# Kernel tuning notes

Measured on AMD Instinct MI355X. Metric: run time of the kernel, lower is better.

Reference implementation:

```python
import jax, jax.numpy as jnp
import numpy as np

B, S, H, D, AD = 64, 200, 4, 256, 256  # batch, max_len, heads, hidden, attribute hidden
HD = D // H  # head dim 64
LN_EPS = 1e-12

PARAM_SHAPES = [
    ('Wq', (D, D)), ('bq', (D,)), ('Wk', (D, D)), ('bk', (D,)), ('Wv', (D, D)), ('bv', (D,)),
    ('Wqp', (D, D)), ('bqp', (D,)), ('Wkp', (D, D)), ('bkp', (D,)),
    ('Waq', (AD, AD)), ('baq', (AD,)), ('Wak', (AD, AD)), ('bak', (AD,)), ('Wav', (AD, AD)), ('bav', (AD,)),
    ('Wqic', (D, AD)), ('bqic', (AD,)), ('Wqci', (AD, D)), ('bqci', (D,)),
    ('Wqpc', (D, AD)), ('bqpc', (AD,)), ('Wqcp', (AD, D)), ('bqcp', (D,)),
    ('Wf1', (S, S)), ('bf1', (S,)), ('Wf2', (S, 1)), ('bf2', (1,)),
    ('Wd', (D, D)), ('bd', (D,)), ('ln_g', (D,)), ('ln_b', (D,)),
    ('Wda', (AD, AD)), ('bda', (AD,)), ('lna_g', (AD,)), ('lna_b', (AD,)),
]


def setup_inputs() -> dict:
    key = jax.random.key(0)
    ks = jax.random.split(key, 8 + len(PARAM_SHAPES))
    inp = {
        'input_tensor': jax.random.normal(ks[0], (B, S, D), jnp.float32),
        'attribute_table': jax.random.normal(ks[1], (1, B, S, 1, AD), jnp.float32),
        'position_embedding': jax.random.normal(ks[2], (B, S, D), jnp.float32),
        'hidden_state_attr': jax.random.normal(ks[3], (1, B, S, 1, AD), jnp.float32),
        'attention_mask': jnp.zeros((B, 1, S, S), jnp.float32),
        'fusion_w': jax.random.uniform(ks[4], (9,), jnp.float32),
        'fusion_wc': jax.random.uniform(ks[5], (4,), jnp.float32),
    }
    for j, (name, shp) in enumerate(PARAM_SHAPES):
        if name.startswith('ln') or name == 'lna_g':
            inp[name] = jnp.ones(shp, jnp.float32) if name.endswith('_g') else jnp.zeros(shp, jnp.float32)
        else:
            inp[name] = jax.random.normal(ks[8 + j], shp, jnp.float32) * 0.02
    return inp


def _forward(input_tensor, attribute_table, position_embedding, hidden_state_attr,
             attention_mask, fusion_w, fusion_wc,
             Wq, bq, Wk, bk, Wv, bv, Wqp, bqp, Wkp, bkp,
             Waq, baq, Wak, bak, Wav, bav, Wqic, bqic, Wqci, bqci,
             Wqpc, bqpc, Wqcp, bqcp, Wf1, bf1, Wf2, bf2,
             Wd, bd, ln_g, ln_b, Wda, bda, lna_g, lna_b):
    lin = lambda x, W, b: x @ W + b

    def heads(x):  # [B,S,D] -> [B,H,S,hd]
        b_, s_, _ = x.shape
        return x.reshape(b_, s_, H, -1).transpose(0, 2, 1, 3)

    def ln(x, g, b):
        m = x.mean(-1, keepdims=True)
        v = ((x - m) ** 2).mean(-1, keepdims=True)
        return (x - m) / jnp.sqrt(v + LN_EPS) * g + b

    attr = attribute_table[0, :, :, 0, :]      # [B,S,AD] (squeeze(-2), feat 0)
    hattr = hidden_state_attr[0, :, :, 0, :]   # [B,S,AD]

    iq, ik, iv = heads(lin(input_tensor, Wq, bq)), heads(lin(input_tensor, Wk, bk)), heads(lin(input_tensor, Wv, bv))
    pq, pk = heads(lin(position_embedding, Wqp, bqp)), heads(lin(position_embedding, Wkp, bkp))
    aq, ak = heads(lin(attr, Waq, baq)), heads(lin(attr, Wak, bak))
    haq, hak, hav = heads(lin(hattr, Waq, baq)), heads(lin(hattr, Wak, bak)), heads(lin(hattr, Wav, bav))
    iqc = heads(lin(input_tensor, Wqic, bqic))
    ciq = heads(lin(attr, Wqci, bqci))
    cqp = heads(lin(attr, Wqcp, bqcp))
    cqp_a = heads(lin(hattr, Wqcp, bqcp))
    pqc = heads(lin(position_embedding, Wqpc, bqpc))

    sc = lambda q, k: jnp.einsum('bhid,bhjd->bhij', q, k)
    pp = sc(pq, pk)
    # 9 item-side streams: ii, ic, ip, ci, cc, cp, pi, pc, pp (matches torch append order)
    raw = jnp.stack([sc(iq, ik), sc(iqc, ak), sc(iq, pk), sc(ciq, ik), sc(aq, ak),
                     sc(cqp, pk), sc(pq, ik), sc(pqc, ak), pp], axis=1)   # [B,9,H,S,S]
    raw_c = jnp.stack([sc(haq, hak), sc(cqp_a, pk), sc(pqc, hak), pp], axis=1)  # [B,4,H,S,S]

    def gate(x, fw):  # VanillaAttention(max_len, max_len) over stream axis
        x = jnp.transpose(x, (0, 2, 3, 1, 4)) * fw[:, None]  # [B,H,S,C,S]
        e = (jax.nn.relu(x @ Wf1 + bf1) @ Wf2 + bf2)[..., 0]  # [B,H,S,C]
        w = jax.nn.softmax(e, axis=-1)
        return jnp.einsum('bhscj,bhsc->bhsj', x, w)  # [B,H,S,S]

    scale = 1.0 / np.sqrt(HD)

    def attend(a, v):
        p = jax.nn.softmax(a * scale + attention_mask, axis=-1)
        ctx = jnp.einsum('bhij,bhjd->bhid', p, v)
        b_ = ctx.shape[0]
        return ctx.transpose(0, 2, 1, 3).reshape(b_, S, -1)

    ctx = attend(gate(raw, fusion_w), iv)
    ctx_c = attend(gate(raw_c, fusion_wc), hav)
    hidden_states = ln(ctx @ Wd + bd + input_tensor, ln_g, ln_b)
    hidden_states_attr = ln(ctx_c @ Wda + bda + hattr, lna_g, lna_b)
    return hidden_states, hidden_states_attr


def reference(input_tensor, attribute_table, position_embedding, hidden_state_attr,
              attention_mask, fusion_w, fusion_wc,
              Wq, bq, Wk, bk, Wv, bv, Wqp, bqp, Wkp, bkp,
              Waq, baq, Wak, bak, Wav, bav, Wqic, bqic, Wqci, bqci,
              Wqpc, bqpc, Wqcp, bqcp, Wf1, bf1, Wf2, bf2,
              Wd, bd, ln_g, ln_b, Wda, bda, lna_g, lna_b):
    return _forward(input_tensor, attribute_table, position_embedding, hidden_state_attr,
                    attention_mask, fusion_w, fusion_wc,
                    Wq, bq, Wk, bk, Wv, bv, Wqp, bqp, Wkp, bkp,
                    Waq, baq, Wak, bak, Wav, bav, Wqic, bqic, Wqci, bqci,
                    Wqpc, bqpc, Wqcp, bqcp, Wf1, bf1, Wf2, bf2,
                    Wd, bd, ln_g, ln_b, Wda, bda, lna_g, lna_b)
```

## Files before the change

kernel.cpp:

```cpp
#include <hip/hip_runtime.h>
#include <cstddef>

typedef __attribute__((ext_vector_type(8))) short bf16x8;
typedef __attribute__((ext_vector_type(4))) short bf16x4;
typedef __attribute__((ext_vector_type(4))) float f32x4;

constexpr int Bc = 64;
constexpr int Sc = 200;
constexpr int Hc = 4;
constexpr int Dc = 256;
constexpr int HDc = 64;
constexpr int NPc = Bc * Sc;
constexpr int NPROJ = 15;
constexpr int NWT   = 17;
constexpr float SCALE = 0.125f;


__constant__ int c_KP9[3]  = {1,6,4};
__constant__ int c_QP9[9]  = {0,11,3, 10,5,14, 0,12,3};
__constant__ int c_CG9[9]  = {0,3,6, 1,4,7, 2,5,8};
__constant__ int c_M2S9[9] = {0,24,48,8,32,56,16,40,64};
__constant__ int c_KP4[2]  = {8,4};
__constant__ int c_QP4[4]  = {7,14, 13,3};
__constant__ int c_CG4[4]  = {0,2, 1,3};
__constant__ int c_M2S4[4] = {0,16,8,24};

__device__ __forceinline__ short f2bf(float x) {
    union { float f; unsigned u; } v; v.f = x;
    unsigned r = v.u + 0x7FFFu + ((v.u >> 16) & 1u);
    return (short)(r >> 16);
}
__device__ __forceinline__ float bf2f(short x) {
    union { unsigned u; float f; } v; v.u = ((unsigned)(unsigned short)x) << 16;
    return v.f;
}
__device__ __forceinline__ f32x4 mfma16(bf16x8 a, bf16x8 b, f32x4 c) {
    return __builtin_amdgcn_mfma_f32_16x16x32_bf16(a, b, c, 0, 0, 0);
}

struct ProjArgsM {
    const short* A[NPROJ];
    const float* bias[NPROJ];
};
struct WList { const float* w[NWT]; };

__global__ void cast_in(const float* __restrict__ s0, const float* __restrict__ s1,
                        const float* __restrict__ s2, const float* __restrict__ s3,
                        short* __restrict__ dst) {
    const float* srcs[4] = {s0, s1, s2, s3};
    const float* src = srcs[blockIdx.y];
    short* d = dst + (size_t)blockIdx.y * NPc * Dc;
    int t = blockIdx.x * 256 + threadIdx.x;
    float4 v = ((const float4*)src)[t];
    bf16x4 o;
    o[0] = f2bf(v.x); o[1] = f2bf(v.y); o[2] = f2bf(v.z); o[3] = f2bf(v.w);
    *(bf16x4*)(d + (size_t)t * 4) = o;
}

__global__ void cast_wt(WList wl, short* __restrict__ dst) {
    __shared__ float tbuf[64][65];
    const int p = blockIdx.y;
    const int k0 = (blockIdx.x >> 2) * 64, n0 = (blockIdx.x & 3) * 64;
    const float* W = wl.w[p];
    short* d = dst + (size_t)p * Dc * Dc;
    const int tid = threadIdx.x;
    for (int i = tid; i < 64 * 64; i += 256) {
        int k = i >> 6, n = i & 63;
        tbuf[k][n] = W[(size_t)(k0 + k) * Dc + n0 + n];
    }
    __syncthreads();
    for (int i = tid; i < 64 * 64; i += 256) {
        int n = i >> 6, k = i & 63;
        d[(size_t)(n0 + n) * Dc + k0 + k] = f2bf(tbuf[k][n]);
    }
}

__global__ void wf1t_kernel(const float* __restrict__ Wf1, short* __restrict__ WT) {
    int t = blockIdx.x * 256 + threadIdx.x;
    if (t < 224 * 224) {
        int j = t / 224, i = t % 224;
        WT[t] = (i < Sc && j < Sc) ? f2bf(Wf1[(size_t)i * Sc + j]) : (short)0;
    }
}

__global__ __launch_bounds__(256) void vt_kernel(const short* __restrict__ proj_bf,
                                                 short* __restrict__ vt) {
    const int bid = blockIdx.x;
    const int t  = bid >> 8;
    const int bh = bid & 255;
    const int b = bh >> 2, h = bh & 3;
    const int p = t ? 9 : 2;
    const short* src = proj_bf + ((size_t)p * NPc + (size_t)b * Sc) * Dc + h * HDc;
    short* dst = vt + ((size_t)t * 256 + bh) * 64 * 224;
    __shared__ short tile[200][72];
    const int tid = threadIdx.x;
    for (int idx = tid; idx < 200 * 8; idx += 256) {
        int j = idx >> 3, c8 = idx & 7;
        *(bf16x8*)(&tile[j][c8 * 8]) = *(const bf16x8*)(src + (size_t)j * Dc + c8 * 8);
    }
    __syncthreads();
    for (int idx = tid; idx < 64 * 28; idx += 256) {
        int d = idx / 28, c8 = idx % 28;
        bf16x8 o;
        #pragma unroll
        for (int i = 0; i < 8; ++i) {
            int j = c8 * 8 + i;
            o[i] = (j < 200) ? tile[j][d] : (short)0;
        }
        *(bf16x8*)(dst + (size_t)d * 224 + c8 * 8) = o;
    }
}

__global__ __launch_bounds__(256, 4) void proj_mfma(
    ProjArgsM args, const short* __restrict__ WTall, short* __restrict__ proj_bf)
{
    const int p  = blockIdx.y;
    const int m0 = blockIdx.x * 64;
    const short* __restrict__ A   = args.A[p];
    const short* __restrict__ WTp = WTall + (size_t)p * Dc * Dc;
    const float* __restrict__ bias = args.bias[p];
    short* __restrict__ ob = proj_bf + (size_t)p * NPc * Dc;

    __shared__ __align__(16) short As[64 * 264];
    const int tid = threadIdx.x;
    const int lane = tid & 63, w = tid >> 6;
    const int l15 = lane & 15, l4 = lane >> 4;

    for (int t = tid; t < 64 * 32; t += 256) {
        int r = t >> 5, c8 = t & 31;
        *(bf16x8*)(As + r * 264 + c8 * 8) = *(const bf16x8*)(A + (size_t)(m0 + r) * Dc + c8 * 8);
    }
    __syncthreads();

    f32x4 acc[4][4];
    #pragma unroll
    for (int mi = 0; mi < 4; ++mi)
        #pragma unroll
        for (int ni = 0; ni < 4; ++ni) acc[mi][ni] = (f32x4){};

    const int nb = w * 64;
    #pragma unroll
    for (int ks = 0; ks < 8; ++ks) {
        bf16x8 bfr[4];
        #pragma unroll
        for (int ni = 0; ni < 4; ++ni)
            bfr[ni] = *(const bf16x8*)(WTp + (size_t)(nb + ni * 16 + l15) * Dc + ks * 32 + l4 * 8);
        #pragma unroll
        for (int mi = 0; mi < 4; ++mi) {
            bf16x8 a = *(const bf16x8*)(As + (mi * 16 + l15) * 264 + ks * 32 + l4 * 8);
            #pragma unroll
            for (int ni = 0; ni < 4; ++ni)
                acc[mi][ni] = mfma16(a, bfr[ni], acc[mi][ni]);
        }
    }

    float bv[4];
    #pragma unroll
    for (int ni = 0; ni < 4; ++ni) bv[ni] = bias[nb + ni * 16 + l15];
    #pragma unroll
    for (int mi = 0; mi < 4; ++mi) {
        #pragma unroll
        for (int ni = 0; ni < 4; ++ni) {
            int n = nb + ni * 16 + l15;
            #pragma unroll
            for (int i = 0; i < 4; ++i) {
                int m = m0 + mi * 16 + l4 * 4 + i;
                ob[(size_t)m * Dc + n] = f2bf(acc[mi][ni][i] + bv[ni]);
            }
        }
    }
}

template <int CH, int NG, int CPG, int QT, int MT2>
__device__ void fused_body(
    int bid,
    const short* __restrict__ proj_bf,
    const short* __restrict__ vtb,
    const float* __restrict__ fw,
    const float* __restrict__ mask,
    const short* __restrict__ WT,
    const float* __restrict__ bf1,
    const float* __restrict__ Wf2,
    short* __restrict__ ctx_out,
    const int* KP, const int* QP, const int* CG, const int* M2S,
    short* Sl, float* gbuf, float* evw, float* fwl,
    float* bf1l, float* wf2l)
{
    constexpr int GR    = CPG * 8;
    constexpr int VROWS = NG * GR;
    constexpr int SROWS = MT2 * 16;
    constexpr int SLD   = 232;
    constexpr int NW    = 4;

    const int tid = threadIdx.x;
    const int rt  = bid % 25;
    const int h   = (bid / 25) & 3;
    const int b   = bid / 100;
    const int r0  = rt * 8;
    const int lane = tid & 63, wv = tid >> 6;
    const int l15 = lane & 15, l4 = lane >> 4;
    const int brow0 = b * Sc + r0;

    {
        bf16x8 z = {};
        if constexpr (SROWS > VROWS) {
            for (int t = tid; t < (SROWS - VROWS) * 28; t += 256) {
                int r = VROWS + t / 28, c8 = t % 28;
                *(bf16x8*)(Sl + r * SLD + c8 * 8) = z;
            }
        }
        for (int t = tid; t < VROWS * 3; t += 256) {
            int r = t / 3, c8 = t % 3;
            *(bf16x8*)(Sl + r * SLD + 200 + c8 * 8) = z;
        }
    }
    if (tid < 224) {
        bf1l[tid] = (tid < Sc) ? bf1[tid] : 0.f;
        wf2l[tid] = (tid < Sc) ? Wf2[tid] : 0.f;
    }
    if (tid < CH) fwl[tid] = fw[tid];

    bf16x8 af[NG][QT][2];
    #pragma unroll
    for (int g = 0; g < NG; ++g) {
        #pragma unroll
        for (int t = 0; t < QT; ++t) {
            int sr = t * 16 + l15;
            int kk = (sr < GR) ? (sr >> 3) : 0;
            int rr = (sr < GR) ? (sr & 7) : 0;
            const short* qp = proj_bf + ((size_t)QP[g * CPG + kk] * NPc + brow0 + rr) * Dc + h * HDc;
            #pragma unroll
            for (int ks = 0; ks < 2; ++ks)
                af[g][t][ks] = *(const bf16x8*)(qp + ks * 32 + l4 * 8);
        }
    }
    __syncthreads();

    {
        const short* Kb[NG];
        #pragma unroll
        for (int g = 0; g < NG; ++g)
            Kb[g] = proj_bf + ((size_t)KP[g] * NPc + (size_t)b * Sc) * Dc + h * HDc;

        float fwv[NG][QT];
        #pragma unroll
        for (int g = 0; g < NG; ++g)
            #pragma unroll
            for (int t = 0; t < QT; ++t) {
                int k = t * 2 + (l4 >> 1);
                fwv[g][t] = (k < CPG) ? fwl[CG[g * CPG + k]] : 0.f;
            }

        bf16x8 cur[NG][2];
        int nt = wv;
        {
            int j = nt * 16 + l15;
            #pragma unroll
            for (int g = 0; g < NG; ++g) {
                cur[g][0] = *(const bf16x8*)(Kb[g] + (size_t)j * Dc + l4 * 8);
                cur[g][1] = *(const bf16x8*)(Kb[g] + (size_t)j * Dc + 32 + l4 * 8);
            }
        }
        while (nt < 13) {
            const int ntn = nt + NW;
            bf16x8 nxt[NG][2];
            if (ntn < 13) {
                int j2 = ntn * 16 + l15;
                #pragma unroll
                for (int g = 0; g < NG; ++g) {
                    nxt[g][0] = *(const bf16x8*)(Kb[g] + (size_t)j2 * Dc + l4 * 8);
                    nxt[g][1] = *(const bf16x8*)(Kb[g] + (size_t)j2 * Dc + 32 + l4 * 8);
                }
            }
            const int j = nt * 16 + l15;
            const bool jv = (j < Sc);
            #pragma unroll
            for (int g = 0; g < NG; ++g) {
                #pragma unroll
                for (int t = 0; t < QT; ++t) {
                    f32x4 c = {};
                    c = mfma16(af[g][t][0], cur[g][0], c);
                    c = mfma16(af[g][t][1], cur[g][1], c);
                    int k = t * 2 + (l4 >> 1);
                    if (jv && k < CPG) {
                        int srb = g * GR + t * 16 + l4 * 4;
                        float f = fwv[g][t];
                        #pragma unroll
                        for (int i = 0; i < 4; ++i)
                            Sl[(srb + i) * SLD + j] = f2bf(c[i] * f);
                    }
                }
            }
            #pragma unroll
            for (int g = 0; g < NG; ++g) { cur[g][0] = nxt[g][0]; cur[g][1] = nxt[g][1]; }
            nt = ntn;
        }
    }
    __syncthreads();

    {
        float epart[MT2];
        #pragma unroll
        for (int mt = 0; mt < MT2; ++mt) epart[mt] = 0.f;

        for (int nt = wv; nt < 13; nt += NW) {
            const int jr = nt * 16 + l15;
            bf16x8 wfrag[7];
            #pragma unroll
            for (int ks = 0; ks < 7; ++ks)
                wfrag[ks] = *(const bf16x8*)(WT + (size_t)jr * 224 + ks * 32 + l4 * 8);
            f32x4 cg[MT2];
            #pragma unroll
            for (int mt = 0; mt < MT2; ++mt) cg[mt] = (f32x4){};
            #pragma unroll
            for (int ks = 0; ks < 7; ++ks) {
                #pragma unroll
                for (int mt = 0; mt < MT2; ++mt) {
                    bf16x8 bb = *(const bf16x8*)(Sl + (mt * 16 + l15) * SLD + ks * 32 + l4 * 8);
                    cg[mt] = mfma16(wfrag[ks], bb, cg[mt]);
                }
            }
            float4 b1 = *(const float4*)(bf1l + nt * 16 + l4 * 4);
            float4 w2 = *(const float4*)(wf2l + nt * 16 + l4 * 4);
            #pragma unroll
            for (int mt = 0; mt < MT2; ++mt) {
                float s = fmaxf(cg[mt][0] + b1.x, 0.f) * w2.x
                        + fmaxf(cg[mt][1] + b1.y, 0.f) * w2.y
                        + fmaxf(cg[mt][2] + b1.z, 0.f) * w2.z
                        + fmaxf(cg[mt][3] + b1.w, 0.f) * w2.w;
                s += __shfl_xor(s, 16, 64);
                s += __shfl_xor(s, 32, 64);
                epart[mt] += s;
            }
        }
        if (l4 == 0) {
            #pragma unroll
            for (int mt = 0; mt < MT2; ++mt)
                evw[wv * SROWS + mt * 16 + l15] = epart[mt];
        }
    }
    __syncthreads();

    const int ra = wv, rb = wv + 4;

    float wchA[CH], wchB[CH];
    {
        float eA[CH], eB[CH];
        float mxA = -1e30f, mxB = -1e30f;
        #pragma unroll
        for (int c = 0; c < CH; ++c) {
            int m = M2S[c];
            float sA = 0.f, sB = 0.f;
            #pragma unroll
            for (int w = 0; w < NW; ++w) {
                sA += evw[w * SROWS + m + ra];
                sB += evw[w * SROWS + m + rb];
            }
            eA[c] = sA; eB[c] = sB;
            mxA = fmaxf(mxA, sA); mxB = fmaxf(mxB, sB);
        }
        float suA = 0.f, suB = 0.f;
        #pragma unroll
        for (int c = 0; c < CH; ++c) {
            eA[c] = __expf(eA[c] - mxA); suA += eA[c];
            eB[c] = __expf(eB[c] - mxB); suB += eB[c];
        }
        float ivA = 1.f / suA, ivB = 1.f / suB;
        #pragma unroll
        for (int c = 0; c < CH; ++c) { wchA[c] = eA[c] * ivA; wchB[c] = eB[c] * ivB; }
    }

    if (lane < 50) {
        const int j4 = lane * 4;
        const float* mbase = mask + ((size_t)b * Sc + r0) * Sc;
        float aA[4] = {0.f, 0.f, 0.f, 0.f};
        float aB[4] = {0.f, 0.f, 0.f, 0.f};
        #pragma unroll
        for (int c = 0; c < CH; ++c) {
            bf16x4 sA = *(const bf16x4*)(Sl + (M2S[c] + ra) * SLD + j4);
            bf16x4 sB = *(const bf16x4*)(Sl + (M2S[c] + rb) * SLD + j4);
            float wA = wchA[c], wB = wchB[c];
            #pragma unroll
            for (int i = 0; i < 4; ++i) {
                aA[i] += wA * bf2f(sA[i]);
                aB[i] += wB * bf2f(sB[i]);
            }
        }
        float4 mA = *(const float4*)(mbase + (size_t)ra * Sc + j4);
        float4 mB = *(const float4*)(mbase + (size_t)rb * Sc + j4);
        float4 oA = make_float4(aA[0] * SCALE + mA.x, aA[1] * SCALE + mA.y,
                                aA[2] * SCALE + mA.z, aA[3] * SCALE + mA.w);
        float4 oB = make_float4(aB[0] * SCALE + mB.x, aB[1] * SCALE + mB.y,
                                aB[2] * SCALE + mB.z, aB[3] * SCALE + mB.w);
        *(float4*)(gbuf + ra * 200 + j4) = oA;
        *(float4*)(gbuf + rb * 200 + j4) = oB;
    }

    #pragma unroll
    for (int rr = 0; rr < 2; ++rr) {
        const int r = wv + rr * 4;
        float vals[4]; float mpart = -1e30f;
        #pragma unroll
        for (int t4 = 0; t4 < 4; ++t4) {
            int j = t4 * 64 + lane;
            vals[t4] = (j < Sc) ? gbuf[r * 200 + j] : -1e30f;
            mpart = fmaxf(mpart, vals[t4]);
        }
        #pragma unroll
        for (int off = 32; off >= 1; off >>= 1) mpart = fmaxf(mpart, __shfl_xor(mpart, off, 64));
        float pv[4]; float spart = 0.f;
        #pragma unroll
        for (int t4 = 0; t4 < 4; ++t4) {
            int j = t4 * 64 + lane;
            pv[t4] = (j < Sc) ? __expf(vals[t4] - mpart) : 0.f;
            spart += pv[t4];
        }
        #pragma unroll
        for (int off = 32; off >= 1; off >>= 1) spart += __shfl_xor(spart, off, 64);
        float inv = 1.f / spart;
        #pragma unroll
        for (int t4 = 0; t4 < 4; ++t4) {
            int j = t4 * 64 + lane;
            if (j < Sc) Sl[r * SLD + j] = f2bf(pv[t4] * inv);
        }
    }
    __syncthreads();

    {
        const short* vb = vtb + ((size_t)(b * Hc + h) * 64) * 224;
        const int nb = wv * 16;
        f32x4 c0 = {}, c1 = {};
        #pragma unroll
        for (int ks = 0; ks < 7; ks += 2) {
            bf16x8 aa = *(const bf16x8*)(Sl + l15 * SLD + ks * 32 + l4 * 8);
            bf16x8 bb = *(const bf16x8*)(vb + (size_t)(nb + l15) * 224 + ks * 32 + l4 * 8);
            c0 = mfma16(aa, bb, c0);
            if (ks + 1 < 7) {
                bf16x8 aa1 = *(const bf16x8*)(Sl + l15 * SLD + (ks + 1) * 32 + l4 * 8);
                bf16x8 bb1 = *(const bf16x8*)(vb + (size_t)(nb + l15) * 224 + (ks + 1) * 32 + l4 * 8);
                c1 = mfma16(aa1, bb1, c1);
            }
        }
        if (l4 < 2) {
            #pragma unroll
            for (int i = 0; i < 4; ++i) {
                int row = l4 * 4 + i;
                ctx_out[((size_t)(brow0 + row)) * Dc + h * HDc + nb + l15] =
                    f2bf(c0[i] + c1[i]);
            }
        }
    }
}

__global__ __launch_bounds__(256, 3) void fused7(
    const short* __restrict__ proj_bf,
    const short* __restrict__ vt,
    const float* __restrict__ fw9,
    const float* __restrict__ fw4,
    const float* __restrict__ mask,
    const short* __restrict__ WT,
    const float* __restrict__ bf1,
    const float* __restrict__ Wf2,
    short* __restrict__ ctxb,
    short* __restrict__ ctxcb)
{
    __shared__ __align__(16) short Sl[80 * 232];
    __shared__ float gbuf[8 * 200];
    __shared__ float evw[4 * 80];
    __shared__ float fwl[9];
    __shared__ float bf1l[224];
    __shared__ float wf2l[224];

    const int d    = blockIdx.x;
    const int xcd  = d & 7;
    const int slot = d >> 3;
    const int chunk = (slot / 25) * 8 + xcd;
    const int pos   = slot % 25;
    const int bid   = chunk * 25 + pos;

    if (bid < 6400) {
        fused_body<9, 3, 3, 2, 5>(bid, proj_bf, vt, fw9, mask, WT, bf1, Wf2, ctxb,
                                  c_KP9, c_QP9, c_CG9, c_M2S9,
                                  Sl, gbuf, evw, fwl, bf1l, wf2l);
    } else {
        fused_body<4, 2, 2, 1, 2>(bid - 6400, proj_bf, vt + (size_t)256 * 64 * 224,
                                  fw4, mask, WT, bf1, Wf2, ctxcb,
                                  c_KP4, c_QP4, c_CG4, c_M2S4,
                                  Sl, gbuf, evw, fwl, bf1l, wf2l);
    }
}

__global__ __launch_bounds__(256, 3) void out_ln_mfma(
    const short* __restrict__ Ab,
    const short* __restrict__ WTp,
    const float* __restrict__ bias,
    const float* __restrict__ resid,
    const float* __restrict__ gamma,
    const float* __restrict__ beta,
    float* __restrict__ out)
{
    const int m0 = blockIdx.x * 32;
    __shared__ __align__(16) short As[32 * 264];
    __shared__ float ylds[32][257];
    const int tid = threadIdx.x;
    const int lane = tid & 63, wv = tid >> 6;
    const int l15 = lane & 15, l4 = lane >> 4;

    for (int t = tid; t < 32 * 32; t += 256) {
        int r = t >> 5, c8 = t & 31;
        *(bf16x8*)(As + r * 264 + c8 * 8) = *(const bf16x8*)(Ab + (size_t)(m0 + r) * Dc + c8 * 8);
    }
    __syncthreads();

    const int nb = wv * 64;
    f32x4 acc[2][4];
    #pragma unroll
    for (int mi = 0; mi < 2; ++mi)
        #pragma unroll
        for (int ni = 0; ni < 4; ++ni) acc[mi][ni] = (f32x4){};

    #pragma unroll
    for (int ks = 0; ks < 8; ++ks) {
        bf16x8 bfr[4];
        #pragma unroll
        for (int ni = 0; ni < 4; ++ni)
            bfr[ni] = *(const bf16x8*)(WTp + (size_t)(nb + ni * 16 + l15) * Dc + ks * 32 + l4 * 8);
        #pragma unroll
        for (int mi = 0; mi < 2; ++mi) {
            bf16x8 a = *(const bf16x8*)(As + (mi * 16 + l15) * 264 + ks * 32 + l4 * 8);
            #pragma unroll
            for (int ni = 0; ni < 4; ++ni)
                acc[mi][ni] = mfma16(a, bfr[ni], acc[mi][ni]);
        }
    }

    #pragma unroll
    for (int mi = 0; mi < 2; ++mi) {
        #pragma unroll
        for (int ni = 0; ni < 4; ++ni) {
            int n = nb + ni * 16 + l15;
            float bv = bias[n];
            #pragma unroll
            for (int i = 0; i < 4; ++i) {
                int row = mi * 16 + l4 * 4 + i;
                ylds[row][n] = acc[mi][ni][i] + bv + resid[(size_t)(m0 + row) * Dc + n];
            }
        }
    }
    __syncthreads();

    for (int r = wv * 8; r < wv * 8 + 8; ++r) {
        float v4[4];
        float s = 0.f, s2 = 0.f;
        #pragma unroll
        for (int t4 = 0; t4 < 4; ++t4) {
            float v = ylds[r][t4 * 64 + lane];
            v4[t4] = v;
            s += v; s2 += v * v;
        }
        #pragma unroll
        for (int off = 32; off >= 1; off >>= 1) {
            s  += __shfl_xor(s, off, 64);
            s2 += __shfl_xor(s2, off, 64);
        }
        float m   = s * (1.f / 256.f);
        float var = s2 * (1.f / 256.f) - m * m;
        float rstd = rsqrtf(var + 1e-12f);
        #pragma unroll
        for (int t4 = 0; t4 < 4; ++t4) {
            int ccol = t4 * 64 + lane;
            out[(size_t)(m0 + r) * Dc + ccol] = (v4[t4] - m) * rstd * gamma[ccol] + beta[ccol];
        }
    }
}

extern "C" void kernel_launch(void* const* d_in, const int* in_sizes, int n_in,
                              void* d_out, int out_size, void* d_ws, size_t ws_size,
                              hipStream_t stream) {
    const float* X    = (const float*)d_in[0];
    const float* AT   = (const float*)d_in[1];
    const float* P    = (const float*)d_in[2];
    const float* HA   = (const float*)d_in[3];
    const float* mask = (const float*)d_in[4];
    const float* fw   = (const float*)d_in[5];
    const float* fwc  = (const float*)d_in[6];

    const float* Wq   = (const float*)d_in[7];
    const float* bq   = (const float*)d_in[8];
    const float* Wk   = (const float*)d_in[9];
    const float* bk   = (const float*)d_in[10];
    const float* Wv   = (const float*)d_in[11];
    const float* bv   = (const float*)d_in[12];
    const float* Wqp  = (const float*)d_in[13];
    const float* bqp  = (const float*)d_in[14];
    const float* Wkp  = (const float*)d_in[15];
    const float* bkp  = (const float*)d_in[16];
    const float* Waq  = (const float*)d_in[17];
    const float* baq  = (const float*)d_in[18];
    const float* Wak  = (const float*)d_in[19];
    const float* bak  = (const float*)d_in[20];
    const float* Wav  = (const float*)d_in[21];
    const float* bav  = (const float*)d_in[22];
    const float* Wqic = (const float*)d_in[23];
    const float* bqic = (const float*)d_in[24];
    const float* Wqci = (const float*)d_in[25];
    const float* bqci = (const float*)d_in[26];
    const float* Wqpc = (const float*)d_in[27];
    const float* bqpc = (const float*)d_in[28];
    const float* Wqcp = (const float*)d_in[29];
    const float* bqcp = (const float*)d_in[30];
    const float* Wf1  = (const float*)d_in[31];
    const float* bf1  = (const float*)d_in[32];
    const float* Wf2  = (const float*)d_in[33];
    const float* bf2  = (const float*)d_in[34];
    const float* Wd   = (const float*)d_in[35];
    const float* bd   = (const float*)d_in[36];
    const float* ln_g = (const float*)d_in[37];
    const float* ln_b = (const float*)d_in[38];
    const float* Wda  = (const float*)d_in[39];
    const float* bda  = (const float*)d_in[40];
    const float* lna_g= (const float*)d_in[41];
    const float* lna_b= (const float*)d_in[42];

    char* w = (char*)d_ws;
    short* proj_bf = (short*)w;  w += (size_t)NPROJ * NPc * Dc * sizeof(short);
    short* WTall   = (short*)w;  w += (size_t)NWT * Dc * Dc * sizeof(short);
    short* WTf1    = (short*)w;  w += (size_t)224 * 224 * sizeof(short);
    short* inb     = (short*)w;  w += (size_t)4 * NPc * Dc * sizeof(short);
    short* vt      = (short*)w;  w += (size_t)2 * 256 * 64 * 224 * sizeof(short);
    short* ctxb    = (short*)w;  w += (size_t)NPc * Dc * sizeof(short);
    short* ctxcb   = (short*)w;  w += (size_t)NPc * Dc * sizeof(short);

    const int aid[NPROJ] = {0,0,0,2,2,1,1,3,3,3,0,1,1,3,2};
    const float* Wmat[NWT] = {Wq, Wk, Wv, Wqp, Wkp, Waq, Wak, Waq, Wak, Wav,
                              Wqic, Wqci, Wqcp, Wqcp, Wqpc, Wd, Wda};
    const float* bmat[NPROJ] = {bq, bk, bv, bqp, bkp, baq, bak, baq, bak, bav,
                                bqic, bqci, bqcp, bqcp, bqpc};

    ProjArgsM pm;
    WList wl;
    for (int i = 0; i < NPROJ; i++) {
        pm.A[i]    = inb + (size_t)aid[i] * NPc * Dc;
        pm.bias[i] = bmat[i];
    }
    for (int i = 0; i < NWT; i++) wl.w[i] = Wmat[i];

    cast_in<<<dim3(NPc * Dc / 4 / 256, 4), 256, 0, stream>>>(X, AT, P, HA, inb);
    cast_wt<<<dim3(16, NWT), 256, 0, stream>>>(wl, WTall);
    wf1t_kernel<<<(224 * 224 + 255) / 256, 256, 0, stream>>>(Wf1, WTf1);

    proj_mfma<<<dim3(NPc / 64, NPROJ), 256, 0, stream>>>(pm, WTall, proj_bf);

    vt_kernel<<<512, 256, 0, stream>>>(proj_bf, vt);

    fused7<<<12800, 256, 0, stream>>>(proj_bf, vt, fw, fwc, mask, WTf1, bf1, Wf2, ctxb, ctxcb);

    float* out0 = (float*)d_out;
    float* out1 = out0 + (size_t)NPc * Dc;
    out_ln_mfma<<<NPc / 32, 256, 0, stream>>>(ctxb,  WTall + (size_t)15 * Dc * Dc, bd,
                                              X,  ln_g,  ln_b,  out0);
    out_ln_mfma<<<NPc / 32, 256, 0, stream>>>(ctxcb, WTall + (size_t)16 * Dc * Dc, bda,
                                              HA, lna_g, lna_b, out1);
}
```

Before: 477.6 us.

## Cut fused attention LDS footprint and compute softmax in registers

Removes the gbuf and evw shared buffers from the fused attention kernel. The per-wave partial sums now go into the padding columns of the score tile, and the softmax runs directly on the register values each lane already holds instead of being staged through shared memory. The kernel's launch bounds are raised from 3 to 4 blocks per CU to use the smaller LDS footprint. It also replaces scalar bf16 rounding with the packed v_cvt_pk_bf16_f32 instruction in several kernels, which trades the hand-written rounding for the hardware conversion's rounding and risks register spills under the tighter bound.

New measurement: 594.1 us. 1.24x slower.

```diff
diff --git a/kernel.cpp b/kernel.cpp
--- a/kernel.cpp
+++ b/kernel.cpp
@@ -13,6 +13,7 @@
 constexpr int NPc = Bc * Sc;
 constexpr int NPROJ = 15;
 constexpr int NWT   = 17;
+constexpr int SLD   = 232;
 constexpr float SCALE = 0.125f;
 
 
@@ -34,6 +35,11 @@
     union { unsigned u; float f; } v; v.u = ((unsigned)(unsigned short)x) << 16;
     return v.f;
 }
+__device__ __forceinline__ unsigned cvtpk(float lo, float hi) {
+    unsigned r;
+    asm("v_cvt_pk_bf16_f32 %0, %1, %2" : "=v"(r) : "v"(lo), "v"(hi));
+    return r;
+}
 __device__ __forceinline__ f32x4 mfma16(bf16x8 a, bf16x8 b, f32x4 c) {
     return __builtin_amdgcn_mfma_f32_16x16x32_bf16(a, b, c, 0, 0, 0);
 }
@@ -52,9 +58,9 @@
     short* d = dst + (size_t)blockIdx.y * NPc * Dc;
     int t = blockIdx.x * 256 + threadIdx.x;
     float4 v = ((const float4*)src)[t];
-    bf16x4 o;
-    o[0] = f2bf(v.x); o[1] = f2bf(v.y); o[2] = f2bf(v.z); o[3] = f2bf(v.w);
-    *(bf16x4*)(d + (size_t)t * 4) = o;
+    unsigned p01 = cvtpk(v.x, v.y), p23 = cvtpk(v.z, v.w);
+    uint2 st; st.x = p01; st.y = p23;
+    *(uint2*)(d + (size_t)t * 4) = st;
 }
 
 __global__ void cast_wt(WList wl, short* __restrict__ dst) {
@@ -162,11 +168,13 @@
         #pragma unroll
         for (int ni = 0; ni < 4; ++ni) {
             int n = nb + ni * 16 + l15;
-            #pragma unroll
-            for (int i = 0; i < 4; ++i) {
-                int m = m0 + mi * 16 + l4 * 4 + i;
-                ob[(size_t)m * Dc + n] = f2bf(acc[mi][ni][i] + bv[ni]);
-            }
+            int m = m0 + mi * 16 + l4 * 4;
+            unsigned p01 = cvtpk(acc[mi][ni][0] + bv[ni], acc[mi][ni][1] + bv[ni]);
+            unsigned p23 = cvtpk(acc[mi][ni][2] + bv[ni], acc[mi][ni][3] + bv[ni]);
+            ob[(size_t)(m + 0) * Dc + n] = (short)p01;
+            ob[(size_t)(m + 1) * Dc + n] = (short)(p01 >> 16);
+            ob[(size_t)(m + 2) * Dc + n] = (short)p23;
+            ob[(size_t)(m + 3) * Dc + n] = (short)(p23 >> 16);
         }
     }
 }
@@ -183,13 +191,11 @@
     const float* __restrict__ Wf2,
     short* __restrict__ ctx_out,
     const int* KP, const int* QP, const int* CG, const int* M2S,
-    short* Sl, float* gbuf, float* evw, float* fwl,
-    float* bf1l, float* wf2l)
+    short* Sl, float* fwl, float* bf1l, float* wf2l)
 {
     constexpr int GR    = CPG * 8;
     constexpr int VROWS = NG * GR;
     constexpr int SROWS = MT2 * 16;
-    constexpr int SLD   = 232;
     constexpr int NW    = 4;
 
     const int tid = threadIdx.x;
@@ -285,9 +291,12 @@
                     if (jv && k < CPG) {
                         int srb = g * GR + t * 16 + l4 * 4;
                         float f = fwv[g][t];
-                        #pragma unroll
-                        for (int i = 0; i < 4; ++i)
-                            Sl[(srb + i) * SLD + j] = f2bf(c[i] * f);
+                        unsigned p01 = cvtpk(c[0] * f, c[1] * f);
+                        unsigned p23 = cvtpk(c[2] * f, c[3] * f);
+                        Sl[(srb + 0) * SLD + j] = (short)p01;
+                        Sl[(srb + 1) * SLD + j] = (short)(p01 >> 16);
+                        Sl[(srb + 2) * SLD + j] = (short)p23;
+                        Sl[(srb + 3) * SLD + j] = (short)(p23 >> 16);
                     }
                 }
             }
@@ -336,7 +345,7 @@
         if (l4 == 0) {
             #pragma unroll
             for (int mt = 0; mt < MT2; ++mt)
-                evw[wv * SROWS + mt * 16 + l15] = epart[mt];
+                *(float*)(Sl + (size_t)(mt * 16 + l15) * SLD + 224 + wv * 2) = epart[mt];
         }
     }
     __syncthreads();
@@ -353,8 +362,8 @@
             float sA = 0.f, sB = 0.f;
             #pragma unroll
             for (int w = 0; w < NW; ++w) {
-                sA += evw[w * SROWS + m + ra];
-                sB += evw[w * SROWS + m + rb];
+                sA += *(const float*)(Sl + (size_t)(m + ra) * SLD + 224 + w * 2);
+                sB += *(const float*)(Sl + (size_t)(m + rb) * SLD + 224 + w * 2);
             }
             eA[c] = sA; eB[c] = sB;
             mxA = fmaxf(mxA, sA); mxB = fmaxf(mxB, sB);
@@ -370,15 +379,17 @@
         for (int c = 0; c < CH; ++c) { wchA[c] = eA[c] * ivA; wchB[c] = eB[c] * ivB; }
     }
 
-    if (lane < 50) {
-        const int j4 = lane * 4;
+    const bool act = lane < 50;
+    const int j4 = lane * 4;
+    float vA[4], vB[4];
+    if (act) {
         const float* mbase = mask + ((size_t)b * Sc + r0) * Sc;
         float aA[4] = {0.f, 0.f, 0.f, 0.f};
         float aB[4] = {0.f, 0.f, 0.f, 0.f};
         #pragma unroll
         for (int c = 0; c < CH; ++c) {
-            bf16x4 sA = *(const bf16x4*)(Sl + (M2S[c] + ra) * SLD + j4);
-            bf16x4 sB = *(const bf16x4*)(Sl + (M2S[c] + rb) * SLD + j4);
+            bf16x4 sA = *(const bf16x4*)(Sl + (size_t)(M2S[c] + ra) * SLD + j4);
+            bf16x4 sB = *(const bf16x4*)(Sl + (size_t)(M2S[c] + rb) * SLD + j4);
             float wA = wchA[c], wB = wchB[c];
             #pragma unroll
             for (int i = 0; i < 4; ++i) {
@@ -388,40 +399,51 @@
         }
         float4 mA = *(const float4*)(mbase + (size_t)ra * Sc + j4);
         float4 mB = *(const float4*)(mbase + (size_t)rb * Sc + j4);
-        float4 oA = make_float4(aA[0] * SCALE + mA.x, aA[1] * SCALE + mA.y,
-                                aA[2] * SCALE + mA.z, aA[3] * SCALE + mA.w);
-        float4 oB = make_float4(aB[0] * SCALE + mB.x, aB[1] * SCALE + mB.y,
-                                aB[2] * SCALE + mB.z, aB[3] * SCALE + mB.w);
-        *(float4*)(gbuf + ra * 200 + j4) = oA;
-        *(float4*)(gbuf + rb * 200 + j4) = oB;
-    }
-
-    #pragma unroll
-    for (int rr = 0; rr < 2; ++rr) {
-        const int r = wv + rr * 4;
-        float vals[4]; float mpart = -1e30f;
-        #pragma unroll
-        for (int t4 = 0; t4 < 4; ++t4) {
-            int j = t4 * 64 + lane;
-            vals[t4] = (j < Sc) ? gbuf[r * 200 + j] : -1e30f;
-            mpart = fmaxf(mpart, vals[t4]);
-        }
-        #pragma unroll
-        for (int off = 32; off >= 1; off >>= 1) mpart = fmaxf(mpart, __shfl_xor(mpart, off, 64));
-        float pv[4]; float spart = 0.f;
-        #pragma unroll
-        for (int t4 = 0; t4 < 4; ++t4) {
-            int j = t4 * 64 + lane;
-            pv[t4] = (j < Sc) ? __expf(vals[t4] - mpart) : 0.f;
-            spart += pv[t4];
-        }
-        #pragma unroll
-        for (int off = 32; off >= 1; off >>= 1) spart += __shfl_xor(spart, off, 64);
-        float inv = 1.f / spart;
-        #pragma unroll
-        for (int t4 = 0; t4 < 4; ++t4) {
-            int j = t4 * 64 + lane;
-            if (j < Sc) Sl[r * SLD + j] = f2bf(pv[t4] * inv);
+        vA[0] = aA[0] * SCALE + mA.x; vA[1] = aA[1] * SCALE + mA.y;
+        vA[2] = aA[2] * SCALE + mA.z; vA[3] = aA[3] * SCALE + mA.w;
+        vB[0] = aB[0] * SCALE + mB.x; vB[1] = aB[1] * SCALE + mB.y;
+        vB[2] = aB[2] * SCALE + mB.z; vB[3] = aB[3] * SCALE + mB.w;
+    } else {
+        #pragma unroll
+        for (int i = 0; i < 4; ++i) { vA[i] = -1e30f; vB[i] = -1e30f; }
+    }
+
+    {
+        float mx = fmaxf(fmaxf(vA[0], vA[1]), fmaxf(vA[2], vA[3]));
+        #pragma unroll
+        for (int off = 32; off >= 1; off >>= 1) mx = fmaxf(mx, __shfl_xor(mx, off, 64));
+        float p0 = act ? __expf(vA[0] - mx) : 0.f;
+        float p1 = act ? __expf(vA[1] - mx) : 0.f;
+        float p2 = act ? __expf(vA[2] - mx) : 0.f;
+        float p3 = act ? __expf(vA[3] - mx) : 0.f;
+        float s = p0 + p1 + p2 + p3;
+        #pragma unroll
+        for (int off = 32; off >= 1; off >>= 1) s += __shfl_xor(s, off, 64);
+        float inv = 1.f / s;
+        if (act) {
+            uint2 st;
+            st.x = cvtpk(p0 * inv, p1 * inv);
+            st.y = cvtpk(p2 * inv, p3 * inv);
+            *(uint2*)(Sl + (size_t)ra * SLD + j4) = st;
+        }
+    }
+    {
+        float mx = fmaxf(fmaxf(vB[0], vB[1]), fmaxf(vB[2], vB[3]));
+        #pragma unroll
+        for (int off = 32; off >= 1; off >>= 1) mx = fmaxf(mx, __shfl_xor(mx, off, 64));
+        float p0 = act ? __expf(vB[0] - mx) : 0.f;
+        float p1 = act ? __expf(vB[1] - mx) : 0.f;
+        float p2 = act ? __expf(vB[2] - mx) : 0.f;
+        float p3 = act ? __expf(vB[3] - mx) : 0.f;
+        float s = p0 + p1 + p2 + p3;
+        #pragma unroll
+        for (int off = 32; off >= 1; off >>= 1) s += __shfl_xor(s, off, 64);
+        float inv = 1.f / s;
+        if (act) {
+            uint2 st;
+            st.x = cvtpk(p0 * inv, p1 * inv);
+            st.y = cvtpk(p2 * inv, p3 * inv);
+            *(uint2*)(Sl + (size_t)rb * SLD + j4) = st;
         }
     }
     __syncthreads();
@@ -452,7 +474,7 @@
     }
 }
 
-__global__ __launch_bounds__(256, 3) void fused7(
+__global__ __launch_bounds__(256, 4) void fused8(
     const short* __restrict__ proj_bf,
     const short* __restrict__ vt,
     const float* __restrict__ fw9,
@@ -464,9 +486,7 @@
     short* __restrict__ ctxb,
     short* __restrict__ ctxcb)
 {
-    __shared__ __align__(16) short Sl[80 * 232];
-    __shared__ float gbuf[8 * 200];
-    __shared__ float evw[4 * 80];
+    __shared__ __align__(16) short Sl[80 * SLD];
     __shared__ float fwl[9];
     __shared__ float bf1l[224];
     __shared__ float wf2l[224];
@@ -481,12 +501,12 @@
     if (bid < 6400) {
         fused_body<9, 3, 3, 2, 5>(bid, proj_bf, vt, fw9, mask, WT, bf1, Wf2, ctxb,
                                   c_KP9, c_QP9, c_CG9, c_M2S9,
-                                  Sl, gbuf, evw, fwl, bf1l, wf2l);
+                                  Sl, fwl, bf1l, wf2l);
     } else {
         fused_body<4, 2, 2, 1, 2>(bid - 6400, proj_bf, vt + (size_t)256 * 64 * 224,
                                   fw4, mask, WT, bf1, Wf2, ctxcb,
                                   c_KP4, c_QP4, c_CG4, c_M2S4,
-                                  Sl, gbuf, evw, fwl, bf1l, wf2l);
+                                  Sl, fwl, bf1l, wf2l);
     }
 }
 
@@ -653,7 +673,7 @@
 
     vt_kernel<<<512, 256, 0, stream>>>(proj_bf, vt);
 
-    fused7<<<12800, 256, 0, stream>>>(proj_bf, vt, fw, fwc, mask, WTf1, bf1, Wf2, ctxb, ctxcb);
+    fused8<<<12800, 256, 0, stream>>>(proj_bf, vt, fw, fwc, mask, WTf1, bf1, Wf2, ctxb, ctxcb);
 
     float* out0 = (float*)d_out;
     float* out1 = out0 + (size_t)NPc * Dc;
```
